# Performance work log

Measured on AMD Instinct MI355X. Metric: run time of the kernel, lower is better.

The kernel has to match this reference:

```python
import jax, jax.numpy as jnp
import numpy as np

D_IN = 1024
D_OUT = 1024

def setup_inputs() -> dict:
    key = jax.random.key(0)
    ks = jax.random.split(key, 7)
    s = 1.0 / np.sqrt(D_IN)
    x = jax.random.normal(ks[0], (4, 2048, D_IN), dtype=jnp.float32)
    Wq = jax.random.uniform(ks[1], (D_IN, D_OUT), jnp.float32, -s, s)
    bq = jax.random.uniform(ks[2], (D_OUT,), jnp.float32, -s, s)
    Wk = jax.random.uniform(ks[3], (D_IN, D_OUT), jnp.float32, -s, s)
    bk = jax.random.uniform(ks[4], (D_OUT,), jnp.float32, -s, s)
    Wv = jax.random.uniform(ks[5], (D_IN, D_OUT), jnp.float32, -s, s)
    bv = jax.random.uniform(ks[6], (D_OUT,), jnp.float32, -s, s)
    return {"x": x, "Wq": Wq, "bq": bq, "Wk": Wk, "bk": bk, "Wv": Wv, "bv": bv}

def reference(x, Wq, bq, Wk, bk, Wv, bv):
    # q,k,v: [B, T, d_out]
    q = x @ Wq + bq
    k = x @ Wk + bk
    v = x @ Wv + bv
    T = x.shape[1]
    scale = 1.0 / jnp.sqrt(jnp.asarray(D_OUT, x.dtype))
    qk = jnp.einsum('btd,bsd->bts', q, k) * scale  # [B, T, T]
    causal = jnp.tril(jnp.ones((T, T), dtype=bool))
    qk = jnp.where(causal, qk, -jnp.inf)
    probs = jax.nn.softmax(qk, axis=-1)
    return jnp.einsum('bts,bsd->btd', probs, v)
```

## Files before the change

### kernel.cpp

```cpp
#include <hip/hip_runtime.h>
#include <cstdint>
#include <cmath>

#define D_MODEL 1024
#define SEQ 2048
#define BATCH 4

typedef short bf16x8 __attribute__((ext_vector_type(8)));
typedef float f32x4 __attribute__((ext_vector_type(4)));

__device__ __forceinline__ short f2bf(float f) {
  union { float f; unsigned int u; } v; v.f = f;
  unsigned int r = (v.u + 0x7FFFu + ((v.u >> 16) & 1u)) >> 16;
  return (short)r;
}

__device__ __forceinline__ float bf2f(short h) {
  union { unsigned int u; float f; } v;
  v.u = ((unsigned int)(unsigned short)h) << 16;
  return v.f;
}

__device__ __forceinline__ f32x4 mfma16(bf16x8 a, bf16x8 b, f32x4 c) {
  return __builtin_amdgcn_mfma_f32_16x16x32_bf16(a, b, c, 0, 0, 0);
}

__device__ __forceinline__ void load_lds16(const void* g, void* l) {
  __builtin_amdgcn_global_load_lds(
      (const __attribute__((address_space(1))) unsigned int*)g,
      (__attribute__((address_space(3))) unsigned int*)l, 16, 0, 0);
}

__global__ __launch_bounds__(256) void convert_x(const float* __restrict__ x,
                                                 short* __restrict__ xb) {
  int i = blockIdx.x * 256 + threadIdx.x;
  float4 f = ((const float4*)x)[i];
  short4 h;
  h.x = f2bf(f.x); h.y = f2bf(f.y); h.z = f2bf(f.z); h.w = f2bf(f.w);
  ((short4*)xb)[i] = h;
}

__global__ __launch_bounds__(256) void transpose_w(const float* __restrict__ Wq,
                                                   const float* __restrict__ Wk,
                                                   const float* __restrict__ Wv,
                                                   short* __restrict__ wt) {
  const int mat = blockIdx.z;
  const float* __restrict__ W = (mat == 0) ? Wq : (mat == 1) ? Wk : Wv;
  short* __restrict__ o = wt + (size_t)mat * (D_MODEL * D_MODEL);
  __shared__ float tile[32][33];
  const int k0 = blockIdx.x * 32, n0 = blockIdx.y * 32;
  const int lx = threadIdx.x & 31, ly = threadIdx.x >> 5;
#pragma unroll
  for (int i = 0; i < 4; ++i) {
    int r = ly + i * 8;
    tile[r][lx] = W[(size_t)(k0 + r) * D_MODEL + n0 + lx];
  }
  __syncthreads();
#pragma unroll
  for (int i = 0; i < 4; ++i) {
    int r = ly + i * 8;
    o[(size_t)(n0 + r) * D_MODEL + k0 + lx] = f2bf(tile[lx][r]);
  }
}

__global__ __launch_bounds__(512) void qkv_gemm(
    const short* __restrict__ xb, const short* __restrict__ wt,
    const float* __restrict__ bq, const float* __restrict__ bk,
    const float* __restrict__ bv, short* __restrict__ qo,
    short* __restrict__ ko, short* __restrict__ vo) {
  const int m0 = blockIdx.x * 256;
  const int n0 = blockIdx.y * 128;
  const int mat = blockIdx.z;
  const short* __restrict__ w = wt + (size_t)mat * (D_MODEL * D_MODEL);
  const float* __restrict__ bias = (mat == 0) ? bq : (mat == 1) ? bk : bv;

  __shared__ short a_lds[256 * 64];
  __shared__ short b_lds[128 * 64];

  const int tid = threadIdx.x;
  const int wid = tid >> 6;
  const int lane = tid & 63;
  const int quad = lane >> 4;
  const int l16 = lane & 15;
  const int wm = (wid >> 1) * 64;
  const int wn = (wid & 1) * 64;

  f32x4 acc[4][4] = {};

  const int r_local = wid * 8 + (lane >> 3);
  const int c_local = (lane & 7) * 8;

  for (int k0 = 0; k0 < D_MODEL; k0 += 64) {
    __syncthreads();
#pragma unroll
    for (int it = 0; it < 4; ++it) {
      const short* srcA = xb + (size_t)(m0 + it * 64 + r_local) * D_MODEL + k0 + c_local;
      load_lds16(srcA, (char*)a_lds + it * 8192 + wid * 1024);
    }
#pragma unroll
    for (int it = 0; it < 2; ++it) {
      const short* srcB = w + (size_t)(n0 + it * 64 + r_local) * D_MODEL + k0 + c_local;
      load_lds16(srcB, (char*)b_lds + it * 8192 + wid * 1024);
    }
    __syncthreads();
#pragma unroll
    for (int kt = 0; kt < 2; ++kt) {
      bf16x8 af[4], bfr[4];
#pragma unroll
      for (int i = 0; i < 4; ++i)
        af[i] = *(const bf16x8*)(a_lds + (wm + i * 16 + l16) * 64 + kt * 32 + quad * 8);
#pragma unroll
      for (int i = 0; i < 4; ++i)
        bfr[i] = *(const bf16x8*)(b_lds + (wn + i * 16 + l16) * 64 + kt * 32 + quad * 8);
#pragma unroll
      for (int i = 0; i < 4; ++i)
#pragma unroll
        for (int j = 0; j < 4; ++j)
          acc[i][j] = mfma16(af[i], bfr[j], acc[i][j]);
    }
  }
#pragma unroll
  for (int i = 0; i < 4; ++i) {
#pragma unroll
    for (int j = 0; j < 4; ++j) {
#pragma unroll
      for (int r = 0; r < 4; ++r) {
        const int mrow = m0 + wm + i * 16 + quad * 4 + r;
        const int ncol = n0 + wn + j * 16 + l16;
        const float val = acc[i][j][r] + bias[ncol];
        const short h = f2bf(val);
        if (mat == 2) {
          const int bb = mrow >> 11;
          const int t = mrow & 2047;
          vo[((size_t)bb * D_MODEL + ncol) * SEQ + t] = h;
        } else if (mat == 0) {
          qo[(size_t)mrow * D_MODEL + ncol] = h;
        } else {
          ko[(size_t)mrow * D_MODEL + ncol] = h;
        }
      }
    }
  }
}

__global__ __launch_bounds__(256) void sgemm(const short* __restrict__ qb,
                                             const short* __restrict__ kb,
                                             short* __restrict__ S) {
  if (blockIdx.y > blockIdx.x) return;
  const int m0 = blockIdx.x * 128;
  const int n0 = blockIdx.y * 128;
  const int b = blockIdx.z;
  const short* __restrict__ qp = qb + (size_t)b * SEQ * D_MODEL;
  const short* __restrict__ kp = kb + (size_t)b * SEQ * D_MODEL;

  __shared__ short a_lds[128 * 64];
  __shared__ short b_lds[128 * 64];

  const int tid = threadIdx.x;
  const int wid = tid >> 6;
  const int lane = tid & 63;
  const int quad = lane >> 4;
  const int l16 = lane & 15;
  const int mw = (wid >> 1) * 64;
  const int nw = (wid & 1) * 64;

  f32x4 acc[4][4] = {};

  const int r_local = wid * 8 + (lane >> 3);
  const int c_local = (lane & 7) * 8;

  for (int k0 = 0; k0 < D_MODEL; k0 += 64) {
    __syncthreads();
#pragma unroll
    for (int it = 0; it < 4; ++it) {
      const short* srcA = qp + (size_t)(m0 + it * 32 + r_local) * D_MODEL + k0 + c_local;
      load_lds16(srcA, (char*)a_lds + (it * 256 + wid * 64) * 16);
      const short* srcB = kp + (size_t)(n0 + it * 32 + r_local) * D_MODEL + k0 + c_local;
      load_lds16(srcB, (char*)b_lds + (it * 256 + wid * 64) * 16);
    }
    __syncthreads();
#pragma unroll
    for (int kt = 0; kt < 2; ++kt) {
      bf16x8 af[4], bfr[4];
#pragma unroll
      for (int i = 0; i < 4; ++i)
        af[i] = *(const bf16x8*)(a_lds + (mw + i * 16 + l16) * 64 + kt * 32 + quad * 8);
#pragma unroll
      for (int i = 0; i < 4; ++i)
        bfr[i] = *(const bf16x8*)(b_lds + (nw + i * 16 + l16) * 64 + kt * 32 + quad * 8);
#pragma unroll
      for (int i = 0; i < 4; ++i)
#pragma unroll
        for (int j = 0; j < 4; ++j)
          acc[i][j] = mfma16(af[i], bfr[j], acc[i][j]);
    }
  }
#pragma unroll
  for (int i = 0; i < 4; ++i) {
#pragma unroll
    for (int j = 0; j < 4; ++j) {
#pragma unroll
      for (int r = 0; r < 4; ++r) {
        const int mrow = m0 + mw + i * 16 + quad * 4 + r;
        const int ncol = n0 + nw + j * 16 + l16;
        S[((size_t)b * SEQ + mrow) * SEQ + ncol] = f2bf(acc[i][j][r] * 0.03125f);
      }
    }
  }
}

__global__ __launch_bounds__(256) void softmax_rows(const short* __restrict__ S,
                                                    short* __restrict__ P) {
  const int row = blockIdx.x;
  const int t = row & (SEQ - 1);
  const int tid = threadIdx.x;
  const short* __restrict__ srow = S + (size_t)row * SEQ;
  short* __restrict__ prow = P + (size_t)row * SEQ;

  __shared__ float red[4];

  float v[8];
#pragma unroll
  for (int i = 0; i < 8; ++i) {
    const int c = tid + i * 256;
    v[i] = (c <= t) ? bf2f(srow[c]) : -1e30f;
  }
  float m = v[0];
#pragma unroll
  for (int i = 1; i < 8; ++i) m = fmaxf(m, v[i]);
#pragma unroll
  for (int o = 32; o; o >>= 1) m = fmaxf(m, __shfl_xor(m, o));
  if ((tid & 63) == 0) red[tid >> 6] = m;
  __syncthreads();
  m = fmaxf(fmaxf(red[0], red[1]), fmaxf(red[2], red[3]));

  float e[8];
  float s = 0.f;
#pragma unroll
  for (int i = 0; i < 8; ++i) {
    e[i] = __expf(v[i] - m);
    s += e[i];
  }
#pragma unroll
  for (int o = 32; o; o >>= 1) s += __shfl_xor(s, o);
  __syncthreads();
  if ((tid & 63) == 0) red[tid >> 6] = s;
  __syncthreads();
  s = red[0] + red[1] + red[2] + red[3];
  const float rinv = 1.0f / s;
  const int nwr = (t >> 8) + 1;
#pragma unroll
  for (int i = 0; i < 8; ++i)
    if (i < nwr) prow[tid + i * 256] = f2bf(e[i] * rinv);
}

__global__ __launch_bounds__(256) void pvgemm(const short* __restrict__ P,
                                              const short* __restrict__ vtb,
                                              float* __restrict__ out) {
  const int n0 = blockIdx.x * 128;
  const int b = blockIdx.y;
  const int m0 = (15 - blockIdx.z) * 128;
  const short* __restrict__ pp = P + (size_t)b * SEQ * SEQ;
  const short* __restrict__ vp = vtb + (size_t)b * D_MODEL * SEQ;
  const int kmax = m0 + 128;

  __shared__ short a_lds[128 * 64];
  __shared__ short b_lds[128 * 64];

  const int tid = threadIdx.x;
  const int wid = tid >> 6;
  const int lane = tid & 63;
  const int quad = lane >> 4;
  const int l16 = lane & 15;
  const int mw = (wid >> 1) * 64;
  const int nw = (wid & 1) * 64;

  f32x4 acc[4][4] = {};

  const int r_local = wid * 8 + (lane >> 3);
  const int c_local = (lane & 7) * 8;

  for (int k0 = 0; k0 < kmax; k0 += 64) {
    __syncthreads();
#pragma unroll
    for (int it = 0; it < 4; ++it) {
      const short* srcA = pp + (size_t)(m0 + it * 32 + r_local) * SEQ + k0 + c_local;
      load_lds16(srcA, (char*)a_lds + (it * 256 + wid * 64) * 16);
      const short* srcB = vp + (size_t)(n0 + it * 32 + r_local) * SEQ + k0 + c_local;
      load_lds16(srcB, (char*)b_lds + (it * 256 + wid * 64) * 16);
    }
    __syncthreads();
#pragma unroll
    for (int kt = 0; kt < 2; ++kt) {
      bf16x8 af[4], bfr[4];
#pragma unroll
      for (int i = 0; i < 4; ++i)
        af[i] = *(const bf16x8*)(a_lds + (mw + i * 16 + l16) * 64 + kt * 32 + quad * 8);
#pragma unroll
      for (int i = 0; i < 4; ++i)
        bfr[i] = *(const bf16x8*)(b_lds + (nw + i * 16 + l16) * 64 + kt * 32 + quad * 8);
#pragma unroll
      for (int i = 0; i < 4; ++i)
#pragma unroll
        for (int j = 0; j < 4; ++j)
          acc[i][j] = mfma16(af[i], bfr[j], acc[i][j]);
    }
  }
#pragma unroll
  for (int i = 0; i < 4; ++i) {
#pragma unroll
    for (int j = 0; j < 4; ++j) {
#pragma unroll
      for (int r = 0; r < 4; ++r) {
        const int mrow = m0 + mw + i * 16 + quad * 4 + r;
        const int ncol = n0 + nw + j * 16 + l16;
        out[((size_t)b * SEQ + mrow) * D_MODEL + ncol] = acc[i][j][r];
      }
    }
  }
}

extern "C" void kernel_launch(void* const* d_in, const int* in_sizes, int n_in,
                              void* d_out, int out_size, void* d_ws, size_t ws_size,
                              hipStream_t stream) {
  (void)in_sizes; (void)n_in; (void)out_size; (void)ws_size;
  const float* x  = (const float*)d_in[0];
  const float* Wq = (const float*)d_in[1];
  const float* bq = (const float*)d_in[2];
  const float* Wk = (const float*)d_in[3];
  const float* bk = (const float*)d_in[4];
  const float* Wv = (const float*)d_in[5];
  const float* bv = (const float*)d_in[6];
  float* out = (float*)d_out;

  char* ws = (char*)d_ws;
  short* xb = (short*)(ws);
  short* wt = (short*)(ws + 16777216);
  short* qo = (short*)(ws + 23068672);
  short* ko = (short*)(ws + 39845888);
  short* vo = (short*)(ws + 56623104);
  short* S  = (short*)(ws + 73400320);
  short* P  = (short*)(ws);

  convert_x<<<dim3(8192), dim3(256), 0, stream>>>(x, xb);
  transpose_w<<<dim3(32, 32, 3), dim3(256), 0, stream>>>(Wq, Wk, Wv, wt);
  qkv_gemm<<<dim3(32, 8, 3), dim3(512), 0, stream>>>(xb, wt, bq, bk, bv, qo, ko, vo);
  sgemm<<<dim3(16, 16, BATCH), dim3(256), 0, stream>>>(qo, ko, S);
  softmax_rows<<<dim3(BATCH * SEQ), dim3(256), 0, stream>>>(S, P);
  pvgemm<<<dim3(8, BATCH, 16), dim3(256), 0, stream>>>(P, vo, out);
}
```

Before: 289.3 us.

## Double-buffer LDS tiles and XOR-swizzle layout in all three GEMM kernels

```diff
diff --git a/kernel.cpp b/kernel.cpp
--- a/kernel.cpp
+++ b/kernel.cpp
@@ -74,8 +74,8 @@
   const short* __restrict__ w = wt + (size_t)mat * (D_MODEL * D_MODEL);
   const float* __restrict__ bias = (mat == 0) ? bq : (mat == 1) ? bk : bv;
 
-  __shared__ short a_lds[256 * 64];
-  __shared__ short b_lds[128 * 64];
+  __shared__ short a_lds[2][256 * 64];
+  __shared__ short b_lds[2][128 * 64];
 
   const int tid = threadIdx.x;
   const int wid = tid >> 6;
@@ -84,34 +84,41 @@
   const int l16 = lane & 15;
   const int wm = (wid >> 1) * 64;
   const int wn = (wid & 1) * 64;
+  const int sw = l16 & 7;
+  const int r_local = wid * 8 + (lane >> 3);
+  const int c_sw = ((lane & 7) ^ (lane >> 3)) * 8;
 
   f32x4 acc[4][4] = {};
 
-  const int r_local = wid * 8 + (lane >> 3);
-  const int c_local = (lane & 7) * 8;
-
+  auto stage = [&](int k0, int buf) {
+#pragma unroll
+    for (int it = 0; it < 4; ++it)
+      load_lds16(xb + (size_t)(m0 + it * 64 + r_local) * D_MODEL + k0 + c_sw,
+                 (char*)a_lds[buf] + it * 8192 + wid * 1024);
+#pragma unroll
+    for (int it = 0; it < 2; ++it)
+      load_lds16(w + (size_t)(n0 + it * 64 + r_local) * D_MODEL + k0 + c_sw,
+                 (char*)b_lds[buf] + it * 8192 + wid * 1024);
+  };
+
+  stage(0, 0);
   for (int k0 = 0; k0 < D_MODEL; k0 += 64) {
+    const int buf = (k0 >> 6) & 1;
     __syncthreads();
-#pragma unroll
-    for (int it = 0; it < 4; ++it) {
-      const short* srcA = xb + (size_t)(m0 + it * 64 + r_local) * D_MODEL + k0 + c_local;
-      load_lds16(srcA, (char*)a_lds + it * 8192 + wid * 1024);
-    }
-#pragma unroll
-    for (int it = 0; it < 2; ++it) {
-      const short* srcB = w + (size_t)(n0 + it * 64 + r_local) * D_MODEL + k0 + c_local;
-      load_lds16(srcB, (char*)b_lds + it * 8192 + wid * 1024);
-    }
-    __syncthreads();
+    if (k0 + 64 < D_MODEL) stage(k0 + 64, buf ^ 1);
+    const short* al = a_lds[buf];
+    const short* bl = b_lds[buf];
 #pragma unroll
     for (int kt = 0; kt < 2; ++kt) {
       bf16x8 af[4], bfr[4];
 #pragma unroll
       for (int i = 0; i < 4; ++i)
-        af[i] = *(const bf16x8*)(a_lds + (wm + i * 16 + l16) * 64 + kt * 32 + quad * 8);
-#pragma unroll
-      for (int i = 0; i < 4; ++i)
-        bfr[i] = *(const bf16x8*)(b_lds + (wn + i * 16 + l16) * 64 + kt * 32 + quad * 8);
+        af[i] = *(const bf16x8*)(al + (wm + i * 16 + l16) * 64 +
+                                 ((kt * 4 + quad) ^ sw) * 8);
+#pragma unroll
+      for (int i = 0; i < 4; ++i)
+        bfr[i] = *(const bf16x8*)(bl + (wn + i * 16 + l16) * 64 +
+                                  ((kt * 4 + quad) ^ sw) * 8);
 #pragma unroll
       for (int i = 0; i < 4; ++i)
 #pragma unroll
@@ -153,8 +160,8 @@
   const short* __restrict__ qp = qb + (size_t)b * SEQ * D_MODEL;
   const short* __restrict__ kp = kb + (size_t)b * SEQ * D_MODEL;
 
-  __shared__ short a_lds[128 * 64];
-  __shared__ short b_lds[128 * 64];
+  __shared__ short a_lds[2][128 * 64];
+  __shared__ short b_lds[2][128 * 64];
 
   const int tid = threadIdx.x;
   const int wid = tid >> 6;
@@ -163,31 +170,40 @@
   const int l16 = lane & 15;
   const int mw = (wid >> 1) * 64;
   const int nw = (wid & 1) * 64;
+  const int sw = l16 & 7;
+  const int r_local = wid * 8 + (lane >> 3);
+  const int c_sw = ((lane & 7) ^ (lane >> 3)) * 8;
 
   f32x4 acc[4][4] = {};
 
-  const int r_local = wid * 8 + (lane >> 3);
-  const int c_local = (lane & 7) * 8;
-
+  auto stage = [&](int k0, int buf) {
+#pragma unroll
+    for (int it = 0; it < 4; ++it) {
+      load_lds16(qp + (size_t)(m0 + it * 32 + r_local) * D_MODEL + k0 + c_sw,
+                 (char*)a_lds[buf] + it * 4096 + wid * 1024);
+      load_lds16(kp + (size_t)(n0 + it * 32 + r_local) * D_MODEL + k0 + c_sw,
+                 (char*)b_lds[buf] + it * 4096 + wid * 1024);
+    }
+  };
+
+  stage(0, 0);
   for (int k0 = 0; k0 < D_MODEL; k0 += 64) {
+    const int buf = (k0 >> 6) & 1;
     __syncthreads();
-#pragma unroll
-    for (int it = 0; it < 4; ++it) {
-      const short* srcA = qp + (size_t)(m0 + it * 32 + r_local) * D_MODEL + k0 + c_local;
-      load_lds16(srcA, (char*)a_lds + (it * 256 + wid * 64) * 16);
-      const short* srcB = kp + (size_t)(n0 + it * 32 + r_local) * D_MODEL + k0 + c_local;
-      load_lds16(srcB, (char*)b_lds + (it * 256 + wid * 64) * 16);
-    }
-    __syncthreads();
+    if (k0 + 64 < D_MODEL) stage(k0 + 64, buf ^ 1);
+    const short* al = a_lds[buf];
+    const short* bl = b_lds[buf];
 #pragma unroll
     for (int kt = 0; kt < 2; ++kt) {
       bf16x8 af[4], bfr[4];
 #pragma unroll
       for (int i = 0; i < 4; ++i)
-        af[i] = *(const bf16x8*)(a_lds + (mw + i * 16 + l16) * 64 + kt * 32 + quad * 8);
-#pragma unroll
-      for (int i = 0; i < 4; ++i)
-        bfr[i] = *(const bf16x8*)(b_lds + (nw + i * 16 + l16) * 64 + kt * 32 + quad * 8);
+        af[i] = *(const bf16x8*)(al + (mw + i * 16 + l16) * 64 +
+                                 ((kt * 4 + quad) ^ sw) * 8);
+#pragma unroll
+      for (int i = 0; i < 4; ++i)
+        bfr[i] = *(const bf16x8*)(bl + (nw + i * 16 + l16) * 64 +
+                                  ((kt * 4 + quad) ^ sw) * 8);
 #pragma unroll
       for (int i = 0; i < 4; ++i)
 #pragma unroll
@@ -264,8 +280,8 @@
   const short* __restrict__ vp = vtb + (size_t)b * D_MODEL * SEQ;
   const int kmax = m0 + 128;
 
-  __shared__ short a_lds[128 * 64];
-  __shared__ short b_lds[128 * 64];
+  __shared__ short a_lds[2][128 * 64];
+  __shared__ short b_lds[2][128 * 64];
 
   const int tid = threadIdx.x;
   const int wid = tid >> 6;
@@ -274,31 +290,40 @@
   const int l16 = lane & 15;
   const int mw = (wid >> 1) * 64;
   const int nw = (wid & 1) * 64;
+  const int sw = l16 & 7;
+  const int r_local = wid * 8 + (lane >> 3);
+  const int c_sw = ((lane & 7) ^ (lane >> 3)) * 8;
 
   f32x4 acc[4][4] = {};
 
-  const int r_local = wid * 8 + (lane >> 3);
-  const int c_local = (lane & 7) * 8;
-
+  auto stage = [&](int k0, int buf) {
+#pragma unroll
+    for (int it = 0; it < 4; ++it) {
+      load_lds16(pp + (size_t)(m0 + it * 32 + r_local) * SEQ + k0 + c_sw,
+                 (char*)a_lds[buf] + it * 4096 + wid * 1024);
+      load_lds16(vp + (size_t)(n0 + it * 32 + r_local) * SEQ + k0 + c_sw,
+                 (char*)b_lds[buf] + it * 4096 + wid * 1024);
+    }
+  };
+
+  stage(0, 0);
   for (int k0 = 0; k0 < kmax; k0 += 64) {
+    const int buf = (k0 >> 6) & 1;
     __syncthreads();
-#pragma unroll
-    for (int it = 0; it < 4; ++it) {
-      const short* srcA = pp + (size_t)(m0 + it * 32 + r_local) * SEQ + k0 + c_local;
-      load_lds16(srcA, (char*)a_lds + (it * 256 + wid * 64) * 16);
-      const short* srcB = vp + (size_t)(n0 + it * 32 + r_local) * SEQ + k0 + c_local;
-      load_lds16(srcB, (char*)b_lds + (it * 256 + wid * 64) * 16);
-    }
-    __syncthreads();
+    if (k0 + 64 < kmax) stage(k0 + 64, buf ^ 1);
+    const short* al = a_lds[buf];
+    const short* bl = b_lds[buf];
 #pragma unroll
     for (int kt = 0; kt < 2; ++kt) {
       bf16x8 af[4], bfr[4];
 #pragma unroll
       for (int i = 0; i < 4; ++i)
-        af[i] = *(const bf16x8*)(a_lds + (mw + i * 16 + l16) * 64 + kt * 32 + quad * 8);
-#pragma unroll
-      for (int i = 0; i < 4; ++i)
-        bfr[i] = *(const bf16x8*)(b_lds + (nw + i * 16 + l16) * 64 + kt * 32 + quad * 8);
+        af[i] = *(const bf16x8*)(al + (mw + i * 16 + l16) * 64 +
+                                 ((kt * 4 + quad) ^ sw) * 8);
+#pragma unroll
+      for (int i = 0; i < 4; ++i)
+        bfr[i] = *(const bf16x8*)(bl + (nw + i * 16 + l16) * 64 +
+                                  ((kt * 4 + quad) ^ sw) * 8);
 #pragma unroll
       for (int i = 0; i < 4; ++i)
 #pragma unroll
```

After: 266.7 us. 1.08x faster.
